# Kernel tuning notes

Measured on AMD Instinct MI355X. Metric: run time of the kernel, lower is better.

Reference implementation:

```python
import jax, jax.numpy as jnp
import numpy as np

B, L, D, Y = 8, 2500, 512, 8921


def setup_inputs() -> dict:
    key = jax.random.key(0)
    k1, k2, k3, k4, k5, k6 = jax.random.split(key, 6)
    x = jax.random.normal(k1, (B, L, D), dtype=jnp.float32)
    target = jax.random.uniform(k2, (B, Y), dtype=jnp.float32)
    text_inputs = jax.random.randint(k3, (B, L), 0, 50000, dtype=jnp.int32)
    # Xavier-uniform-like init for the two [Y, D] weights
    lim = float(np.sqrt(6.0 / (Y + D)))
    U_weight = jax.random.uniform(k4, (Y, D), dtype=jnp.float32, minval=-lim, maxval=lim)
    final_weight = jax.random.uniform(k5, (Y, D), dtype=jnp.float32, minval=-lim, maxval=lim)
    final_bias = jax.random.uniform(k6, (Y,), dtype=jnp.float32, minval=-0.05, maxval=0.05)
    return {"x": x, "target": target, "text_inputs": text_inputs,
            "U_weight": U_weight, "final_weight": final_weight, "final_bias": final_bias}


def reference(x, target, text_inputs, U_weight, final_weight, final_bias):
    # att: [B, Y, L] = U.weight @ x^T
    att = jnp.einsum('yd,bld->byl', U_weight, x)
    # softmax over sequence dim
    alpha = jax.nn.softmax(att, axis=2)
    # per-label context: [B, Y, D]
    m = jnp.einsum('byl,bld->byd', alpha, x)
    # gated reduction instead of a linear layer: [B, Y]
    y = jnp.einsum('byd,yd->by', m, final_weight) + final_bias
    # BCEWithLogitsLoss (mean over all elements), numerically stable
    loss = jnp.mean(jnp.maximum(y, 0.0) - y * target + jnp.log1p(jnp.exp(-jnp.abs(y))))
    return (y, loss)
```

## Files before the change

### kernel.cpp

```cpp
#include <hip/hip_runtime.h>
#include <stdint.h>

#define B_ 8
#define L_ 2500
#define D_ 512
#define Y_ 8921
#define LP 2560
#define YP 8960
#define BLK 128
#define BK 32
#define NKT 16
#define NS 4
#define LTS 5
#define NBLK (70 * B_ * NS)
#define PERX (NBLK / 8)

typedef float f32x4 __attribute__((ext_vector_type(4)));
typedef __bf16 bf16x8 __attribute__((ext_vector_type(8)));
typedef unsigned short u16;
typedef unsigned int u32;

__device__ __forceinline__ u32 pack2(float a, float b) {
  u32 ua = __float_as_uint(a); ua = (ua + 0x7FFFu + ((ua >> 16) & 1u)) >> 16;
  u32 ub = __float_as_uint(b); ub = (ub + 0x7FFFu + ((ub >> 16) & 1u)) >> 16;
  return ua | (ub << 16);
}

__global__ void cvt_x_kernel(const float* __restrict__ x, u16* __restrict__ xb) {
  int idx = blockIdx.x * 256 + threadIdx.x;
  int row = idx >> 6;
  int c8  = (idx & 63) << 3;
  int b = row / LP;
  int l = row - b * LP;
  uint4 o;
  if (l < L_) {
    const float* s = x + (size_t)(b * L_ + l) * D_ + c8;
    float4 f0 = *(const float4*)s;
    float4 f1 = *(const float4*)(s + 4);
    o.x = pack2(f0.x, f0.y); o.y = pack2(f0.z, f0.w);
    o.z = pack2(f1.x, f1.y); o.w = pack2(f1.z, f1.w);
  } else {
    o = make_uint4(0u, 0u, 0u, 0u);
  }
  *(uint4*)(xb + (size_t)row * D_ + c8) = o;
}

__global__ void cvt_w_kernel(const float* __restrict__ U, const float* __restrict__ Wf,
                             u16* __restrict__ Ub, u16* __restrict__ Wb) {
  int idx = blockIdx.x * 256 + threadIdx.x;
  const int half = YP * 64;
  const float* src = U; u16* dst = Ub;
  int i = idx;
  if (idx >= half) { i -= half; src = Wf; dst = Wb; }
  int row = i >> 6;
  int c8  = (i & 63) << 3;
  uint4 o;
  if (row < Y_) {
    const float* s = src + (size_t)row * D_ + c8;
    float4 f0 = *(const float4*)s;
    float4 f1 = *(const float4*)(s + 4);
    o.x = pack2(f0.x, f0.y); o.y = pack2(f0.z, f0.w);
    o.z = pack2(f1.x, f1.y); o.w = pack2(f1.z, f1.w);
  } else {
    o = make_uint4(0u, 0u, 0u, 0u);
  }
  *(uint4*)(dst + (size_t)row * D_ + c8) = o;
}

__device__ __forceinline__ void async16(const u16* g, u16* l) {
  __builtin_amdgcn_global_load_lds(
      (const __attribute__((address_space(1))) u32*)g,
      (__attribute__((address_space(3))) u32*)l, 16, 0, 0);
}

__global__ __launch_bounds__(256, 2) void fused_kernel(
    const u16* __restrict__ xb,
    const u16* __restrict__ Ub,
    const u16* __restrict__ Wb,
    float* __restrict__ part)
{
  __shared__ __align__(16) u16 sX[BLK * BK];

  const int t    = threadIdx.x;
  const int lane = t & 63;
  const int wv   = t >> 6;
  const int l16  = lane & 15;
  const int q    = lane >> 4;

  const int bid = blockIdx.x;
  const int w   = (bid & 7) * PERX + (bid >> 3);
  const int yt  = w >> 5;
  const int rem = w & 31;
  const int b   = rem >> 2;
  const int s   = rem & 3;
  const int y0  = yt * BLK;

  const int srow = t >> 2;
  const int scol = (t & 3) << 3;
  const u16* gXb = xb + (size_t)b * LP * D_ + (size_t)srow * D_ + scol;
  u16* lX0 = sX + t * 8;
  u16* lX1 = sX + 2048 + t * 8;

  const u16* fU0 = Ub + (size_t)(y0 + wv * 32 + l16) * D_ + q * 8;
  const u16* fU1 = fU0 + (size_t)16 * D_;
  const u16* fW0 = Wb + (size_t)(y0 + wv * 32 + l16) * D_ + q * 8;
  const u16* fW1 = fW0 + (size_t)16 * D_;

  float M[8], Z[8], W[8];
#pragma unroll
  for (int i = 0; i < 8; ++i) { M[i] = -1e30f; Z[i] = 0.f; W[i] = 0.f; }

  const f32x4 z4 = {0.f, 0.f, 0.f, 0.f};

  for (int ltl = 0; ltl < LTS; ++ltl) {
    const int l0 = (s * LTS + ltl) * BLK;
    const u16* gX0 = gXb + (size_t)l0 * D_;
    const u16* gX1 = gX0 + (size_t)64 * D_;

    f32x4 accA[2][8], accS[2][8];
#pragma unroll
    for (int ry = 0; ry < 2; ++ry)
#pragma unroll
      for (int cl = 0; cl < 8; ++cl) { accA[ry][cl] = z4; accS[ry][cl] = z4; }

#pragma unroll 1
    for (int kt = 0; kt < NKT; ++kt) {
      const int ko = kt * BK;
      bf16x8 aU0 = *(const bf16x8*)(const void*)(fU0 + ko);
      bf16x8 aU1 = *(const bf16x8*)(const void*)(fU1 + ko);
      bf16x8 aW0 = *(const bf16x8*)(const void*)(fW0 + ko);
      bf16x8 aW1 = *(const bf16x8*)(const void*)(fW1 + ko);
      __syncthreads();
      async16(gX0 + ko, lX0);
      async16(gX1 + ko, lX1);
      __syncthreads();

#pragma unroll
      for (int cl = 0; cl < 8; ++cl) {
        bf16x8 bX = *(const bf16x8*)(const void*)(sX + (cl * 16 + l16) * BK + q * 8);
        accA[0][cl] = __builtin_amdgcn_mfma_f32_16x16x32_bf16(aU0, bX, accA[0][cl], 0, 0, 0);
        accA[1][cl] = __builtin_amdgcn_mfma_f32_16x16x32_bf16(aU1, bX, accA[1][cl], 0, 0, 0);
        accS[0][cl] = __builtin_amdgcn_mfma_f32_16x16x32_bf16(aW0, bX, accS[0][cl], 0, 0, 0);
        accS[1][cl] = __builtin_amdgcn_mfma_f32_16x16x32_bf16(aW1, bX, accS[1][cl], 0, 0, 0);
      }
    }

    const bool boundary = (l0 + BLK > L_);
#pragma unroll
    for (int ry = 0; ry < 2; ++ry) {
#pragma unroll
      for (int r = 0; r < 4; ++r) {
        const int si = ry * 4 + r;
        float a[8];
        if (boundary) {
#pragma unroll
          for (int cl = 0; cl < 8; ++cl) {
            float v = accA[ry][cl][r];
            a[cl] = (l0 + cl * 16 + l16 >= L_) ? -1e30f : v;
          }
        } else {
#pragma unroll
          for (int cl = 0; cl < 8; ++cl) a[cl] = accA[ry][cl][r];
        }
        float tmax = a[0];
#pragma unroll
        for (int cl = 1; cl < 8; ++cl) tmax = fmaxf(tmax, a[cl]);
        const float mnew  = fmaxf(M[si], tmax);
        const float scale = __expf(M[si] - mnew);
        float zl = 0.f, wl = 0.f;
#pragma unroll
        for (int cl = 0; cl < 8; ++cl) {
          float p = __expf(a[cl] - mnew);
          zl += p;
          wl = fmaf(p, accS[ry][cl][r], wl);
        }
        Z[si] = fmaf(Z[si], scale, zl);
        W[si] = fmaf(W[si], scale, wl);
        M[si] = mnew;
      }
    }
  }

#pragma unroll
  for (int si = 0; si < 8; ++si) {
    float M0 = M[si], Z0 = Z[si], W0 = W[si];
#pragma unroll
    for (int st = 1; st <= 8; st <<= 1) {
      const float Mo = __shfl_xor(M0, st);
      const float Zo = __shfl_xor(Z0, st);
      const float Wo = __shfl_xor(W0, st);
      const float mn = fmaxf(M0, Mo);
      const float sa = __expf(M0 - mn);
      const float sb = __expf(Mo - mn);
      Z0 = Z0 * sa + Zo * sb;
      W0 = W0 * sa + Wo * sb;
      M0 = mn;
    }
    M[si] = M0; Z[si] = Z0; W[si] = W0;
  }

  if (l16 == 0) {
    float* p = part + ((size_t)(b * 70 + yt) * NS + s) * 384;
#pragma unroll
    for (int ry = 0; ry < 2; ++ry) {
#pragma unroll
      for (int r = 0; r < 4; ++r) {
        const int si = ry * 4 + r;
        const int yl = wv * 32 + ry * 16 + q * 4 + r;
        p[yl]       = M[si];
        p[128 + yl] = Z[si];
        p[256 + yl] = W[si];
      }
    }
  }
}

__global__ void combine_kernel(const float* __restrict__ part,
                               const float* __restrict__ bias,
                               const float* __restrict__ target,
                               float* __restrict__ out) {
  const int idx = blockIdx.x * 256 + threadIdx.x;
  float lpart = 0.f;
  if (idx < B_ * Y_) {
    const int b = idx / Y_;
    const int y = idx - b * Y_;
    const int yt = y >> 7, yl = y & 127;
    const float* p = part + ((size_t)(b * 70 + yt) * NS) * 384 + yl;
    float M = -1e30f;
#pragma unroll
    for (int s2 = 0; s2 < NS; ++s2) M = fmaxf(M, p[s2 * 384]);
    float Z = 0.f, W = 0.f;
#pragma unroll
    for (int s2 = 0; s2 < NS; ++s2) {
      const float e = __expf(p[s2 * 384] - M);
      Z = fmaf(p[s2 * 384 + 128], e, Z);
      W = fmaf(p[s2 * 384 + 256], e, W);
    }
    const float yv = W / Z + bias[y];
    out[idx] = yv;
    const float tg = target[idx];
    lpart = fmaxf(yv, 0.f) - yv * tg + log1pf(__expf(-fabsf(yv)));
  }
  lpart += __shfl_xor(lpart, 1);  lpart += __shfl_xor(lpart, 2);
  lpart += __shfl_xor(lpart, 4);  lpart += __shfl_xor(lpart, 8);
  lpart += __shfl_xor(lpart, 16); lpart += __shfl_xor(lpart, 32);
  if ((threadIdx.x & 63) == 0)
    atomicAdd(out + (size_t)B_ * Y_, lpart * (1.0f / (B_ * Y_)));
}

extern "C" void kernel_launch(void* const* d_in, const int* in_sizes, int n_in,
                              void* d_out, int out_size, void* d_ws, size_t ws_size,
                              hipStream_t stream) {
  const float* x      = (const float*)d_in[0];
  const float* target = (const float*)d_in[1];
  const float* U      = (const float*)d_in[3];
  const float* Wf     = (const float*)d_in[4];
  const float* bias   = (const float*)d_in[5];
  float* out = (float*)d_out;

  u16* xb = (u16*)d_ws;
  u16* Ub = xb + (size_t)B_ * LP * D_;
  u16* Wb = Ub + (size_t)YP * D_;
  float* part = (float*)(Wb + (size_t)YP * D_);

  hipMemsetAsync(out + (size_t)B_ * Y_, 0, sizeof(float), stream);
  cvt_x_kernel<<<dim3((B_ * LP * 64) / 256), 256, 0, stream>>>(x, xb);
  cvt_w_kernel<<<dim3((2 * YP * 64) / 256), 256, 0, stream>>>(U, Wf, Ub, Wb);
  fused_kernel<<<dim3(NBLK), 256, 0, stream>>>(xb, Ub, Wb, part);
  combine_kernel<<<dim3((B_ * Y_ + 255) / 256), 256, 0, stream>>>(part, bias, target, out);
}
```

Before: 604.0 us.

## Halve label tile per block and split columns across wave pairs

Shrinks the label tile per block from 128 to 64 and has pairs of waves split the 128 sequence columns, so each wave keeps half as many accumulators. Occupancy is raised to 3 blocks per CU. The two halves' softmax partials are merged through shared memory before being written. The x tile load is also issued before the weight-fragment loads so they overlap. The cost is twice as many blocks and twice as much x traffic from global/L2, since each x tile is now reused by only 64 labels.

```diff
diff --git a/kernel.cpp b/kernel.cpp
--- a/kernel.cpp
+++ b/kernel.cpp
@@ -7,12 +7,14 @@
 #define Y_ 8921
 #define LP 2560
 #define YP 8960
+#define YT 64
 #define BLK 128
 #define BK 32
 #define NKT 16
 #define NS 4
 #define LTS 5
-#define NBLK (70 * B_ * NS)
+#define NYT 140
+#define NBLK (NYT * B_ * NS)
 #define PERX (NBLK / 8)
 
 typedef float f32x4 __attribute__((ext_vector_type(4)));
@@ -73,17 +75,20 @@
       (__attribute__((address_space(3))) u32*)l, 16, 0, 0);
 }
 
-__global__ __launch_bounds__(256, 2) void fused_kernel(
+__global__ __launch_bounds__(256, 3) void fused_kernel(
     const u16* __restrict__ xb,
     const u16* __restrict__ Ub,
     const u16* __restrict__ Wb,
     float* __restrict__ part)
 {
   __shared__ __align__(16) u16 sX[BLK * BK];
+  __shared__ float sMZW[3 * YT];
 
   const int t    = threadIdx.x;
   const int lane = t & 63;
   const int wv   = t >> 6;
+  const int wv2  = wv >> 1;
+  const int ch   = wv & 1;
   const int l16  = lane & 15;
   const int q    = lane >> 4;
 
@@ -93,7 +98,7 @@
   const int rem = w & 31;
   const int b   = rem >> 2;
   const int s   = rem & 3;
-  const int y0  = yt * BLK;
+  const int y0  = yt * YT;
 
   const int srow = t >> 2;
   const int scol = (t & 3) << 3;
@@ -101,9 +106,9 @@
   u16* lX0 = sX + t * 8;
   u16* lX1 = sX + 2048 + t * 8;
 
-  const u16* fU0 = Ub + (size_t)(y0 + wv * 32 + l16) * D_ + q * 8;
+  const u16* fU0 = Ub + (size_t)(y0 + wv2 * 32 + l16) * D_ + q * 8;
   const u16* fU1 = fU0 + (size_t)16 * D_;
-  const u16* fW0 = Wb + (size_t)(y0 + wv * 32 + l16) * D_ + q * 8;
+  const u16* fW0 = Wb + (size_t)(y0 + wv2 * 32 + l16) * D_ + q * 8;
   const u16* fW1 = fW0 + (size_t)16 * D_;
 
   float M[8], Z[8], W[8];
@@ -117,27 +122,27 @@
     const u16* gX0 = gXb + (size_t)l0 * D_;
     const u16* gX1 = gX0 + (size_t)64 * D_;
 
-    f32x4 accA[2][8], accS[2][8];
+    f32x4 accA[2][4], accS[2][4];
 #pragma unroll
     for (int ry = 0; ry < 2; ++ry)
 #pragma unroll
-      for (int cl = 0; cl < 8; ++cl) { accA[ry][cl] = z4; accS[ry][cl] = z4; }
+      for (int cl = 0; cl < 4; ++cl) { accA[ry][cl] = z4; accS[ry][cl] = z4; }
 
 #pragma unroll 1
     for (int kt = 0; kt < NKT; ++kt) {
       const int ko = kt * BK;
+      __syncthreads();
+      async16(gX0 + ko, lX0);
+      async16(gX1 + ko, lX1);
       bf16x8 aU0 = *(const bf16x8*)(const void*)(fU0 + ko);
       bf16x8 aU1 = *(const bf16x8*)(const void*)(fU1 + ko);
       bf16x8 aW0 = *(const bf16x8*)(const void*)(fW0 + ko);
       bf16x8 aW1 = *(const bf16x8*)(const void*)(fW1 + ko);
       __syncthreads();
-      async16(gX0 + ko, lX0);
-      async16(gX1 + ko, lX1);
-      __syncthreads();
-
-#pragma unroll
-      for (int cl = 0; cl < 8; ++cl) {
-        bf16x8 bX = *(const bf16x8*)(const void*)(sX + (cl * 16 + l16) * BK + q * 8);
+
+#pragma unroll
+      for (int cl = 0; cl < 4; ++cl) {
+        bf16x8 bX = *(const bf16x8*)(const void*)(sX + ((ch * 4 + cl) * 16 + l16) * BK + q * 8);
         accA[0][cl] = __builtin_amdgcn_mfma_f32_16x16x32_bf16(aU0, bX, accA[0][cl], 0, 0, 0);
         accA[1][cl] = __builtin_amdgcn_mfma_f32_16x16x32_bf16(aU1, bX, accA[1][cl], 0, 0, 0);
         accS[0][cl] = __builtin_amdgcn_mfma_f32_16x16x32_bf16(aW0, bX, accS[0][cl], 0, 0, 0);
@@ -151,25 +156,23 @@
 #pragma unroll
       for (int r = 0; r < 4; ++r) {
         const int si = ry * 4 + r;
-        float a[8];
+        float a[4];
         if (boundary) {
 #pragma unroll
-          for (int cl = 0; cl < 8; ++cl) {
+          for (int cl = 0; cl < 4; ++cl) {
             float v = accA[ry][cl][r];
-            a[cl] = (l0 + cl * 16 + l16 >= L_) ? -1e30f : v;
+            a[cl] = (l0 + (ch * 4 + cl) * 16 + l16 >= L_) ? -1e30f : v;
           }
         } else {
 #pragma unroll
-          for (int cl = 0; cl < 8; ++cl) a[cl] = accA[ry][cl][r];
+          for (int cl = 0; cl < 4; ++cl) a[cl] = accA[ry][cl][r];
         }
-        float tmax = a[0];
-#pragma unroll
-        for (int cl = 1; cl < 8; ++cl) tmax = fmaxf(tmax, a[cl]);
+        float tmax = fmaxf(fmaxf(a[0], a[1]), fmaxf(a[2], a[3]));
         const float mnew  = fmaxf(M[si], tmax);
         const float scale = __expf(M[si] - mnew);
         float zl = 0.f, wl = 0.f;
 #pragma unroll
-        for (int cl = 0; cl < 8; ++cl) {
+        for (int cl = 0; cl < 4; ++cl) {
           float p = __expf(a[cl] - mnew);
           zl += p;
           wl = fmaf(p, accS[ry][cl][r], wl);
@@ -199,17 +202,37 @@
     M[si] = M0; Z[si] = Z0; W[si] = W0;
   }
 
-  if (l16 == 0) {
-    float* p = part + ((size_t)(b * 70 + yt) * NS + s) * 384;
-#pragma unroll
-    for (int ry = 0; ry < 2; ++ry) {
+  __syncthreads();
+  if (ch == 1 && l16 == 0) {
+#pragma unroll
+    for (int ry = 0; ry < 2; ++ry)
 #pragma unroll
       for (int r = 0; r < 4; ++r) {
         const int si = ry * 4 + r;
-        const int yl = wv * 32 + ry * 16 + q * 4 + r;
-        p[yl]       = M[si];
-        p[128 + yl] = Z[si];
-        p[256 + yl] = W[si];
+        const int yl = wv2 * 32 + ry * 16 + q * 4 + r;
+        sMZW[yl]            = M[si];
+        sMZW[YT + yl]       = Z[si];
+        sMZW[2 * YT + yl]   = W[si];
+      }
+  }
+  __syncthreads();
+  if (ch == 0 && l16 == 0) {
+    float* p = part + ((size_t)(b * NYT + yt) * NS + s) * 192;
+#pragma unroll
+    for (int ry = 0; ry < 2; ++ry) {
+#pragma unroll
+      for (int r = 0; r < 4; ++r) {
+        const int si = ry * 4 + r;
+        const int yl = wv2 * 32 + ry * 16 + q * 4 + r;
+        const float Mo = sMZW[yl];
+        const float Zo = sMZW[YT + yl];
+        const float Wo = sMZW[2 * YT + yl];
+        const float mn = fmaxf(M[si], Mo);
+        const float sa = __expf(M[si] - mn);
+        const float sb = __expf(Mo - mn);
+        p[yl]        = mn;
+        p[64 + yl]   = Z[si] * sa + Zo * sb;
+        p[128 + yl]  = W[si] * sa + Wo * sb;
       }
     }
   }
@@ -224,17 +247,17 @@
   if (idx < B_ * Y_) {
     const int b = idx / Y_;
     const int y = idx - b * Y_;
-    const int yt = y >> 7, yl = y & 127;
-    const float* p = part + ((size_t)(b * 70 + yt) * NS) * 384 + yl;
+    const int yt = y >> 6, yl = y & 63;
+    const float* p = part + ((size_t)(b * NYT + yt) * NS) * 192 + yl;
     float M = -1e30f;
 #pragma unroll
-    for (int s2 = 0; s2 < NS; ++s2) M = fmaxf(M, p[s2 * 384]);
+    for (int s2 = 0; s2 < NS; ++s2) M = fmaxf(M, p[s2 * 192]);
     float Z = 0.f, W = 0.f;
 #pragma unroll
     for (int s2 = 0; s2 < NS; ++s2) {
-      const float e = __expf(p[s2 * 384] - M);
-      Z = fmaf(p[s2 * 384 + 128], e, Z);
-      W = fmaf(p[s2 * 384 + 256], e, W);
+      const float e = __expf(p[s2 * 192] - M);
+      Z = fmaf(p[s2 * 192 + 64], e, Z);
+      W = fmaf(p[s2 * 192 + 128], e, W);
     }
     const float yv = W / Z + bias[y];
     out[idx] = yv;
```

Result: slower. 885.4 us (+46.6%).

## Load X fragments directly from global, drop LDS staging and barriers

Applied to the files above, without the earlier changes.

Each wave now reads its X fragments straight from global memory into registers instead of staging them through LDS with async loads and two barriers per k-step. MFMA groups are wrapped in s_setprio, and the block-to-work mapping is changed so the 8 blocks sharing a blockIdx group cover different (b,s) combos of the same y tile. The goal is to remove barrier stalls and LDS traffic. In exchange, each of the four waves re-reads the same X data from global/L2, which raises cache bandwidth demand.

```diff
diff --git a/kernel.cpp b/kernel.cpp
--- a/kernel.cpp
+++ b/kernel.cpp
@@ -67,20 +67,12 @@
   *(uint4*)(dst + (size_t)row * D_ + c8) = o;
 }
 
-__device__ __forceinline__ void async16(const u16* g, u16* l) {
-  __builtin_amdgcn_global_load_lds(
-      (const __attribute__((address_space(1))) u32*)g,
-      (__attribute__((address_space(3))) u32*)l, 16, 0, 0);
-}
-
 __global__ __launch_bounds__(256, 2) void fused_kernel(
     const u16* __restrict__ xb,
     const u16* __restrict__ Ub,
     const u16* __restrict__ Wb,
     float* __restrict__ part)
 {
-  __shared__ __align__(16) u16 sX[BLK * BK];
-
   const int t    = threadIdx.x;
   const int lane = t & 63;
   const int wv   = t >> 6;
@@ -88,34 +80,30 @@
   const int q    = lane >> 4;
 
   const int bid = blockIdx.x;
-  const int w   = (bid & 7) * PERX + (bid >> 3);
-  const int yt  = w >> 5;
-  const int rem = w & 31;
-  const int b   = rem >> 2;
-  const int s   = rem & 3;
+  const int i   = bid >> 3;
+  const int c4  = i / 70;
+  const int yt  = i - c4 * 70;
+  const int combo = (bid & 7) * 4 + c4;
+  const int b   = combo >> 2;
+  const int s   = combo & 3;
   const int y0  = yt * BLK;
-
-  const int srow = t >> 2;
-  const int scol = (t & 3) << 3;
-  const u16* gXb = xb + (size_t)b * LP * D_ + (size_t)srow * D_ + scol;
-  u16* lX0 = sX + t * 8;
-  u16* lX1 = sX + 2048 + t * 8;
 
   const u16* fU0 = Ub + (size_t)(y0 + wv * 32 + l16) * D_ + q * 8;
   const u16* fU1 = fU0 + (size_t)16 * D_;
   const u16* fW0 = Wb + (size_t)(y0 + wv * 32 + l16) * D_ + q * 8;
   const u16* fW1 = fW0 + (size_t)16 * D_;
 
+  const u16* xbase = xb + ((size_t)b * LP + l16) * D_ + q * 8;
+
   float M[8], Z[8], W[8];
 #pragma unroll
-  for (int i = 0; i < 8; ++i) { M[i] = -1e30f; Z[i] = 0.f; W[i] = 0.f; }
+  for (int ii = 0; ii < 8; ++ii) { M[ii] = -1e30f; Z[ii] = 0.f; W[ii] = 0.f; }
 
   const f32x4 z4 = {0.f, 0.f, 0.f, 0.f};
 
   for (int ltl = 0; ltl < LTS; ++ltl) {
     const int l0 = (s * LTS + ltl) * BLK;
-    const u16* gX0 = gXb + (size_t)l0 * D_;
-    const u16* gX1 = gX0 + (size_t)64 * D_;
+    const u16* xq0 = xbase + (size_t)l0 * D_;
 
     f32x4 accA[2][8], accS[2][8];
 #pragma unroll
@@ -130,19 +118,33 @@
       bf16x8 aU1 = *(const bf16x8*)(const void*)(fU1 + ko);
       bf16x8 aW0 = *(const bf16x8*)(const void*)(fW0 + ko);
       bf16x8 aW1 = *(const bf16x8*)(const void*)(fW1 + ko);
-      __syncthreads();
-      async16(gX0 + ko, lX0);
-      async16(gX1 + ko, lX1);
-      __syncthreads();
-
-#pragma unroll
-      for (int cl = 0; cl < 8; ++cl) {
-        bf16x8 bX = *(const bf16x8*)(const void*)(sX + (cl * 16 + l16) * BK + q * 8);
-        accA[0][cl] = __builtin_amdgcn_mfma_f32_16x16x32_bf16(aU0, bX, accA[0][cl], 0, 0, 0);
-        accA[1][cl] = __builtin_amdgcn_mfma_f32_16x16x32_bf16(aU1, bX, accA[1][cl], 0, 0, 0);
-        accS[0][cl] = __builtin_amdgcn_mfma_f32_16x16x32_bf16(aW0, bX, accS[0][cl], 0, 0, 0);
-        accS[1][cl] = __builtin_amdgcn_mfma_f32_16x16x32_bf16(aW1, bX, accS[1][cl], 0, 0, 0);
-      }
+
+      bf16x8 xf[4];
+#pragma unroll
+      for (int cl = 0; cl < 4; ++cl)
+        xf[cl] = *(const bf16x8*)(const void*)(xq0 + (size_t)cl * 16 * D_ + ko);
+      __builtin_amdgcn_s_setprio(1);
+#pragma unroll
+      for (int cl = 0; cl < 4; ++cl) {
+        accA[0][cl] = __builtin_amdgcn_mfma_f32_16x16x32_bf16(aU0, xf[cl], accA[0][cl], 0, 0, 0);
+        accA[1][cl] = __builtin_amdgcn_mfma_f32_16x16x32_bf16(aU1, xf[cl], accA[1][cl], 0, 0, 0);
+        accS[0][cl] = __builtin_amdgcn_mfma_f32_16x16x32_bf16(aW0, xf[cl], accS[0][cl], 0, 0, 0);
+        accS[1][cl] = __builtin_amdgcn_mfma_f32_16x16x32_bf16(aW1, xf[cl], accS[1][cl], 0, 0, 0);
+      }
+      __builtin_amdgcn_s_setprio(0);
+
+#pragma unroll
+      for (int cl = 0; cl < 4; ++cl)
+        xf[cl] = *(const bf16x8*)(const void*)(xq0 + (size_t)(cl + 4) * 16 * D_ + ko);
+      __builtin_amdgcn_s_setprio(1);
+#pragma unroll
+      for (int cl = 0; cl < 4; ++cl) {
+        accA[0][cl + 4] = __builtin_amdgcn_mfma_f32_16x16x32_bf16(aU0, xf[cl], accA[0][cl + 4], 0, 0, 0);
+        accA[1][cl + 4] = __builtin_amdgcn_mfma_f32_16x16x32_bf16(aU1, xf[cl], accA[1][cl + 4], 0, 0, 0);
+        accS[0][cl + 4] = __builtin_amdgcn_mfma_f32_16x16x32_bf16(aW0, xf[cl], accS[0][cl + 4], 0, 0, 0);
+        accS[1][cl + 4] = __builtin_amdgcn_mfma_f32_16x16x32_bf16(aW1, xf[cl], accS[1][cl + 4], 0, 0, 0);
+      }
+      __builtin_amdgcn_s_setprio(0);
     }
 
     const bool boundary = (l0 + BLK > L_);
```

Result: slower. 1.088 ms (+80.1%).

## Restructure fused kernel into 2D-tiled double-buffered LDS pipeline with 512 threads

Applied to the files above, without the earlier changes.

The fused attention kernel moves from 256-thread blocks, where each wave streams its own U/W fragments from global memory, to 512-thread blocks that stage U, W and X tiles into LDS through a double-buffered async pipeline. Each block now covers a 128x256 (Y x L) tile with a 2x4 wave grid, and partial softmax statistics are merged across waves in shared memory. The grid grows to 10 L-splits per (b, y-tile), so the combine kernel reads more partials. The aim is to cut redundant global loads of the weights, overlap loads with MFMA work, and improve operand reuse, at the cost of more LDS use, heavier register pressure and extra partial traffic.

```diff
diff --git a/kernel.cpp b/kernel.cpp
--- a/kernel.cpp
+++ b/kernel.cpp
@@ -7,13 +7,14 @@
 #define Y_ 8921
 #define LP 2560
 #define YP 8960
-#define BLK 128
+#define BY 128
+#define BL 256
 #define BK 32
 #define NKT 16
-#define NS 4
-#define LTS 5
-#define NBLK (70 * B_ * NS)
+#define NSP 10
+#define NBLK (70 * B_ * NSP)
 #define PERX (NBLK / 8)
+#define BUF 16384
 
 typedef float f32x4 __attribute__((ext_vector_type(4)));
 typedef __bf16 bf16x8 __attribute__((ext_vector_type(8)));
@@ -73,116 +74,119 @@
       (__attribute__((address_space(3))) u32*)l, 16, 0, 0);
 }
 
-__global__ __launch_bounds__(256, 2) void fused_kernel(
+__global__ __launch_bounds__(512, 2) void fused_kernel(
     const u16* __restrict__ xb,
     const u16* __restrict__ Ub,
     const u16* __restrict__ Wb,
     float* __restrict__ part)
 {
-  __shared__ __align__(16) u16 sX[BLK * BK];
+  __shared__ __align__(16) u16 sB[2 * BUF];
+  __shared__ float sSt[3 * 4 * BY];
 
   const int t    = threadIdx.x;
   const int lane = t & 63;
   const int wv   = t >> 6;
+  const int wy   = wv >> 2;
+  const int wl   = wv & 3;
   const int l16  = lane & 15;
   const int q    = lane >> 4;
 
   const int bid = blockIdx.x;
   const int w   = (bid & 7) * PERX + (bid >> 3);
-  const int yt  = w >> 5;
-  const int rem = w & 31;
-  const int b   = rem >> 2;
-  const int s   = rem & 3;
-  const int y0  = yt * BLK;
+  const int yt  = w / 80;
+  const int rem = w - yt * 80;
+  const int b   = rem / NSP;
+  const int s   = rem - b * NSP;
+  const int y0  = yt * BY;
+  const int l0  = s * BL;
 
   const int srow = t >> 2;
   const int scol = (t & 3) << 3;
-  const u16* gXb = xb + (size_t)b * LP * D_ + (size_t)srow * D_ + scol;
-  u16* lX0 = sX + t * 8;
-  u16* lX1 = sX + 2048 + t * 8;
-
-  const u16* fU0 = Ub + (size_t)(y0 + wv * 32 + l16) * D_ + q * 8;
-  const u16* fU1 = fU0 + (size_t)16 * D_;
-  const u16* fW0 = Wb + (size_t)(y0 + wv * 32 + l16) * D_ + q * 8;
-  const u16* fW1 = fW0 + (size_t)16 * D_;
-
-  float M[8], Z[8], W[8];
-#pragma unroll
-  for (int i = 0; i < 8; ++i) { M[i] = -1e30f; Z[i] = 0.f; W[i] = 0.f; }
+  const u16* gU  = Ub + (size_t)(y0 + srow) * D_ + scol;
+  const u16* gW  = Wb + (size_t)(y0 + srow) * D_ + scol;
+  const u16* gX0 = xb + ((size_t)b * LP + l0 + srow) * D_ + scol;
+  const u16* gX1 = gX0 + (size_t)128 * D_;
+
+  const int offU = (wy * 64 + l16) * BK + q * 8;
+  const int offX = 8192 + (wl * 64 + l16) * BK + q * 8;
+
+  auto stage = [&](int kt, int buf) {
+    u16* base = sB + buf * BUF;
+    const int ko = kt * BK;
+    async16(gU + ko,  base + t * 8);
+    async16(gW + ko,  base + 4096 + t * 8);
+    async16(gX0 + ko, base + 8192 + t * 8);
+    async16(gX1 + ko, base + 12288 + t * 8);
+  };
 
   const f32x4 z4 = {0.f, 0.f, 0.f, 0.f};
-
-  for (int ltl = 0; ltl < LTS; ++ltl) {
-    const int l0 = (s * LTS + ltl) * BLK;
-    const u16* gX0 = gXb + (size_t)l0 * D_;
-    const u16* gX1 = gX0 + (size_t)64 * D_;
-
-    f32x4 accA[2][8], accS[2][8];
-#pragma unroll
-    for (int ry = 0; ry < 2; ++ry)
-#pragma unroll
-      for (int cl = 0; cl < 8; ++cl) { accA[ry][cl] = z4; accS[ry][cl] = z4; }
-
+  f32x4 accA[4][4], accS[4][4];
+#pragma unroll
+  for (int yi = 0; yi < 4; ++yi)
+#pragma unroll
+    for (int xi = 0; xi < 4; ++xi) { accA[yi][xi] = z4; accS[yi][xi] = z4; }
+
+  stage(0, 0);
 #pragma unroll 1
-    for (int kt = 0; kt < NKT; ++kt) {
-      const int ko = kt * BK;
-      bf16x8 aU0 = *(const bf16x8*)(const void*)(fU0 + ko);
-      bf16x8 aU1 = *(const bf16x8*)(const void*)(fU1 + ko);
-      bf16x8 aW0 = *(const bf16x8*)(const void*)(fW0 + ko);
-      bf16x8 aW1 = *(const bf16x8*)(const void*)(fW1 + ko);
-      __syncthreads();
-      async16(gX0 + ko, lX0);
-      async16(gX1 + ko, lX1);
-      __syncthreads();
-
-#pragma unroll
-      for (int cl = 0; cl < 8; ++cl) {
-        bf16x8 bX = *(const bf16x8*)(const void*)(sX + (cl * 16 + l16) * BK + q * 8);
-        accA[0][cl] = __builtin_amdgcn_mfma_f32_16x16x32_bf16(aU0, bX, accA[0][cl], 0, 0, 0);
-        accA[1][cl] = __builtin_amdgcn_mfma_f32_16x16x32_bf16(aU1, bX, accA[1][cl], 0, 0, 0);
-        accS[0][cl] = __builtin_amdgcn_mfma_f32_16x16x32_bf16(aW0, bX, accS[0][cl], 0, 0, 0);
-        accS[1][cl] = __builtin_amdgcn_mfma_f32_16x16x32_bf16(aW1, bX, accS[1][cl], 0, 0, 0);
-      }
-    }
-
-    const bool boundary = (l0 + BLK > L_);
-#pragma unroll
-    for (int ry = 0; ry < 2; ++ry) {
-#pragma unroll
-      for (int r = 0; r < 4; ++r) {
-        const int si = ry * 4 + r;
-        float a[8];
-        if (boundary) {
-#pragma unroll
-          for (int cl = 0; cl < 8; ++cl) {
-            float v = accA[ry][cl][r];
-            a[cl] = (l0 + cl * 16 + l16 >= L_) ? -1e30f : v;
-          }
-        } else {
-#pragma unroll
-          for (int cl = 0; cl < 8; ++cl) a[cl] = accA[ry][cl][r];
-        }
-        float tmax = a[0];
-#pragma unroll
-        for (int cl = 1; cl < 8; ++cl) tmax = fmaxf(tmax, a[cl]);
-        const float mnew  = fmaxf(M[si], tmax);
-        const float scale = __expf(M[si] - mnew);
-        float zl = 0.f, wl = 0.f;
-#pragma unroll
-        for (int cl = 0; cl < 8; ++cl) {
-          float p = __expf(a[cl] - mnew);
-          zl += p;
-          wl = fmaf(p, accS[ry][cl][r], wl);
-        }
-        Z[si] = fmaf(Z[si], scale, zl);
-        W[si] = fmaf(W[si], scale, wl);
-        M[si] = mnew;
-      }
-    }
-  }
-
-#pragma unroll
-  for (int si = 0; si < 8; ++si) {
+  for (int kt = 0; kt < NKT; ++kt) {
+    const int cur = kt & 1;
+    if (kt + 1 < NKT) {
+      stage(kt + 1, cur ^ 1);
+      asm volatile("s_waitcnt vmcnt(4)" ::: "memory");
+    } else {
+      asm volatile("s_waitcnt vmcnt(0)" ::: "memory");
+    }
+    __builtin_amdgcn_s_barrier();
+    asm volatile("" ::: "memory");
+
+    const u16* bb = sB + cur * BUF;
+    bf16x8 xf[4];
+#pragma unroll
+    for (int xi = 0; xi < 4; ++xi)
+      xf[xi] = *(const bf16x8*)(const void*)(bb + offX + xi * 16 * BK);
+    __builtin_amdgcn_s_setprio(1);
+#pragma unroll
+    for (int yi = 0; yi < 4; ++yi) {
+      bf16x8 aU = *(const bf16x8*)(const void*)(bb + offU + yi * 16 * BK);
+      bf16x8 aW = *(const bf16x8*)(const void*)(bb + 4096 + offU + yi * 16 * BK);
+#pragma unroll
+      for (int xi = 0; xi < 4; ++xi) {
+        accA[yi][xi] = __builtin_amdgcn_mfma_f32_16x16x32_bf16(aU, xf[xi], accA[yi][xi], 0, 0, 0);
+        accS[yi][xi] = __builtin_amdgcn_mfma_f32_16x16x32_bf16(aW, xf[xi], accS[yi][xi], 0, 0, 0);
+      }
+    }
+    __builtin_amdgcn_s_setprio(0);
+    asm volatile("" ::: "memory");
+    __builtin_amdgcn_s_barrier();
+  }
+
+  float M[16], Z[16], W[16];
+  const bool boundary = (l0 + BL > L_);
+#pragma unroll
+  for (int yi = 0; yi < 4; ++yi) {
+#pragma unroll
+    for (int r = 0; r < 4; ++r) {
+      const int si = yi * 4 + r;
+      float a[4];
+#pragma unroll
+      for (int xi = 0; xi < 4; ++xi) {
+        float v = accA[yi][xi][r];
+        a[xi] = (boundary && (l0 + wl * 64 + xi * 16 + l16 >= L_)) ? -1e30f : v;
+      }
+      const float mx = fmaxf(fmaxf(a[0], a[1]), fmaxf(a[2], a[3]));
+      float zl = 0.f, wl_ = 0.f;
+#pragma unroll
+      for (int xi = 0; xi < 4; ++xi) {
+        const float p = __expf(a[xi] - mx);
+        zl += p;
+        wl_ = fmaf(p, accS[yi][xi][r], wl_);
+      }
+      M[si] = mx; Z[si] = zl; W[si] = wl_;
+    }
+  }
+
+#pragma unroll
+  for (int si = 0; si < 16; ++si) {
     float M0 = M[si], Z0 = Z[si], W0 = W[si];
 #pragma unroll
     for (int st = 1; st <= 8; st <<= 1) {
@@ -199,19 +203,36 @@
     M[si] = M0; Z[si] = Z0; W[si] = W0;
   }
 
+  __syncthreads();
   if (l16 == 0) {
-    float* p = part + ((size_t)(b * 70 + yt) * NS + s) * 384;
-#pragma unroll
-    for (int ry = 0; ry < 2; ++ry) {
+#pragma unroll
+    for (int yi = 0; yi < 4; ++yi) {
 #pragma unroll
       for (int r = 0; r < 4; ++r) {
-        const int si = ry * 4 + r;
-        const int yl = wv * 32 + ry * 16 + q * 4 + r;
-        p[yl]       = M[si];
-        p[128 + yl] = Z[si];
-        p[256 + yl] = W[si];
-      }
-    }
+        const int si = yi * 4 + r;
+        const int yloc = wy * 64 + yi * 16 + q * 4 + r;
+        sSt[wl * BY + yloc]        = M[si];
+        sSt[512 + wl * BY + yloc]  = Z[si];
+        sSt[1024 + wl * BY + yloc] = W[si];
+      }
+    }
+  }
+  __syncthreads();
+  if (t < BY) {
+    float Mm = sSt[t];
+#pragma unroll
+    for (int k = 1; k < 4; ++k) Mm = fmaxf(Mm, sSt[k * BY + t]);
+    float Zm = 0.f, Wm = 0.f;
+#pragma unroll
+    for (int k = 0; k < 4; ++k) {
+      const float e = __expf(sSt[k * BY + t] - Mm);
+      Zm = fmaf(sSt[512 + k * BY + t], e, Zm);
+      Wm = fmaf(sSt[1024 + k * BY + t], e, Wm);
+    }
+    float* p = part + ((size_t)(b * 70 + yt) * NSP + s) * 384;
+    p[t]       = Mm;
+    p[128 + t] = Zm;
+    p[256 + t] = Wm;
   }
 }
 
@@ -225,13 +246,13 @@
     const int b = idx / Y_;
     const int y = idx - b * Y_;
     const int yt = y >> 7, yl = y & 127;
-    const float* p = part + ((size_t)(b * 70 + yt) * NS) * 384 + yl;
+    const float* p = part + ((size_t)(b * 70 + yt) * NSP) * 384 + yl;
     float M = -1e30f;
 #pragma unroll
-    for (int s2 = 0; s2 < NS; ++s2) M = fmaxf(M, p[s2 * 384]);
+    for (int s2 = 0; s2 < NSP; ++s2) M = fmaxf(M, p[s2 * 384]);
     float Z = 0.f, W = 0.f;
 #pragma unroll
-    for (int s2 = 0; s2 < NS; ++s2) {
+    for (int s2 = 0; s2 < NSP; ++s2) {
       const float e = __expf(p[s2 * 384] - M);
       Z = fmaf(p[s2 * 384 + 128], e, Z);
       W = fmaf(p[s2 * 384 + 256], e, W);
@@ -266,6 +287,6 @@
   hipMemsetAsync(out + (size_t)B_ * Y_, 0, sizeof(float), stream);
   cvt_x_kernel<<<dim3((B_ * LP * 64) / 256), 256, 0, stream>>>(x, xb);
   cvt_w_kernel<<<dim3((2 * YP * 64) / 256), 256, 0, stream>>>(U, Wf, Ub, Wb);
-  fused_kernel<<<dim3(NBLK), 256, 0, stream>>>(xb, Ub, Wb, part);
+  fused_kernel<<<dim3(NBLK), 512, 0, stream>>>(xb, Ub, Wb, part);
   combine_kernel<<<dim3((B_ * Y_ + 255) / 256), 256, 0, stream>>>(part, bias, target, out);
 }
```

New measurement: 674.1 us. 1.12x slower.
